# Kernel tuning notes

Measured on AMD Instinct MI355X. Metric: run time of the kernel, lower is better.

The kernel has to match this reference:

```python
import jax, jax.numpy as jnp
import numpy as np

B, N, D, H = 2, 2048, 2048, 16
HD = D // H  # head_dim = 128


def _rope(x, cos, sin):
    # x: [B,H,N,HD]; cos/sin: [N,HD]. use_real=True, use_real_unbind_dim=-1 (interleaved pairs).
    xr = x[..., 0::2]
    xi = x[..., 1::2]
    x_rot = jnp.stack([-xi, xr], axis=-1).reshape(x.shape)
    return x * cos[None, None] + x_rot * sin[None, None]


def setup_inputs() -> dict:
    key = jax.random.key(0)
    ks = jax.random.split(key, 10)
    x = jax.random.normal(ks[0], (B, N, D), dtype=jnp.float32)
    # realistic RoPE tables
    inv_freq = 1.0 / (10000.0 ** (np.arange(0, HD, 2, dtype=np.float32) / HD))
    t = np.arange(N, dtype=np.float32)
    ang = np.einsum('n,f->nf', t, inv_freq)           # [N, HD/2]
    ang = np.repeat(ang, 2, axis=-1)                  # [N, HD] interleaved
    cos = jnp.asarray(np.cos(ang))
    sin = jnp.asarray(np.sin(ang))
    s = 0.02
    Wq = jax.random.normal(ks[1], (D, D), dtype=jnp.float32) * s
    Wk = jax.random.normal(ks[2], (D, D), dtype=jnp.float32) * s
    Wv = jax.random.normal(ks[3], (D, D), dtype=jnp.float32) * s
    Wo = jax.random.normal(ks[4], (D, D), dtype=jnp.float32) * s
    bq = jnp.zeros((D,), jnp.float32)
    bk = jnp.zeros((D,), jnp.float32)
    bv = jnp.zeros((D,), jnp.float32)
    bo = jnp.zeros((D,), jnp.float32)
    return {"x": x, "cos": cos, "sin": sin, "Wq": Wq, "bq": bq, "Wk": Wk,
            "bk": bk, "Wv": Wv, "bv": bv, "Wo": Wo, "bo": bo}


def reference(x, cos, sin, Wq, bq, Wk, bk, Wv, bv, Wo, bo):
    scale = HD ** -0.5
    q = x @ Wq + bq
    k = x @ Wk + bk
    v = x @ Wv + bv
    # b n (h c) -> b h n c
    def split_heads(t):
        return t.reshape(B, N, H, HD).transpose(0, 2, 1, 3)
    q, k, v = split_heads(q), split_heads(k), split_heads(v)
    q = q * scale  # module's dp_scale
    q = _rope(q, cos, sin)
    k = _rope(k, cos, sin)
    # flash_attn_func(softmax_scale=None) applies head_dim^-0.5 AGAIN -> effective HD^-1
    logits = jnp.einsum('bhqc,bhkc->bhqk', q, k) * scale
    attn = jax.nn.softmax(logits, axis=-1)
    o = jnp.einsum('bhqk,bhkc->bhqc', attn, v)
    o = o.transpose(0, 2, 1, 3).reshape(B, N, D)  # b h n c -> b n (h c)
    return o @ Wo + bo
```

## Files before the change

### kernel.cpp

```cpp
#include <hip/hip_runtime.h>

typedef unsigned short u16;
typedef unsigned int u32;
typedef __attribute__((ext_vector_type(8))) short bfx8;
typedef __attribute__((ext_vector_type(4))) float fx4;
typedef __attribute__((ext_vector_type(16))) float fx16;
typedef __attribute__((ext_vector_type(4))) unsigned short u16x4;

#define MFMA_BF16(a,b,c)   __builtin_amdgcn_mfma_f32_16x16x32_bf16((a),(b),(c),0,0,0)
#define MFMA32_BF16(a,b,c) __builtin_amdgcn_mfma_f32_32x32x16_bf16((a),(b),(c),0,0,0)

#define BATCH 2
#define SEQ   2048
#define DM    2048
#define NH    16
#define HD    128
#define MR    4096

__device__ __forceinline__ u16 f2bf(float f){
  union{float f; unsigned u;} v; v.f = f;
  unsigned r = v.u + 0x7FFFu + ((v.u >> 16) & 1u);
  return (u16)(r >> 16);
}
__device__ __forceinline__ unsigned cvtpk(float lo, float hi){
  unsigned r;
  asm("v_cvt_pk_bf16_f32 %0, %1, %2" : "=v"(r) : "v"(lo), "v"(hi));
  return r;
}
__device__ __forceinline__ void gll16(const void* g, void* l){
  __builtin_amdgcn_global_load_lds(
      (const __attribute__((address_space(1))) void*)g,
      (__attribute__((address_space(3))) void*)l, 16, 0, 0);
}

__global__ __launch_bounds__(256) void k_cast(const float* __restrict__ in,
                                              u16* __restrict__ o, int n4){
  int gid = blockIdx.x*256 + threadIdx.x;
  if (gid >= n4) return;
  float4 x = ((const float4*)in)[gid];
  u16x4 v = {f2bf(x.x), f2bf(x.y), f2bf(x.z), f2bf(x.w)};
  ((u16x4*)o)[gid] = v;
}

__global__ __launch_bounds__(256) void k_twcat(const float* __restrict__ Wq,
                                               const float* __restrict__ Wk,
                                               const float* __restrict__ Wv,
                                               u16* __restrict__ Th){
  __shared__ float T[64][65];
  int z = blockIdx.z;
  const float* W = (z==0) ? Wq : (z==1) ? Wk : Wv;
  int n0 = blockIdx.x*64, k0 = blockIdx.y*64;
  int t = threadIdx.x;
  int r = t>>2, c = (t&3)*16;
  const float* src = W + (size_t)(k0+r)*DM + n0 + c;
  #pragma unroll
  for (int j=0;j<4;j++){
    float4 v = *(const float4*)(src + 4*j);
    T[r][c+4*j+0]=v.x; T[r][c+4*j+1]=v.y; T[r][c+4*j+2]=v.z; T[r][c+4*j+3]=v.w;
  }
  __syncthreads();
  int nr = t>>2, kc = (t&3)*16;
  size_t ob = (size_t)(z*DM + n0+nr)*DM + k0 + kc;
  #pragma unroll
  for (int j=0;j<16;j+=4){
    u16x4 vh;
    #pragma unroll
    for (int q=0;q<4;q++) vh[q] = f2bf(T[kc+j+q][nr]);
    *(u16x4*)(Th+ob+j)=vh;
  }
}

__global__ __launch_bounds__(256) void k_tw(const float* __restrict__ W, u16* __restrict__ Th){
  __shared__ float T[64][65];
  int n0 = blockIdx.x*64, k0 = blockIdx.y*64;
  int t = threadIdx.x;
  int r = t>>2, c = (t&3)*16;
  const float* src = W + (size_t)(k0+r)*DM + n0 + c;
  #pragma unroll
  for (int j=0;j<4;j++){
    float4 v = *(const float4*)(src + 4*j);
    T[r][c+4*j+0]=v.x; T[r][c+4*j+1]=v.y; T[r][c+4*j+2]=v.z; T[r][c+4*j+3]=v.w;
  }
  __syncthreads();
  int nr = t>>2, kc = (t&3)*16;
  size_t ob = (size_t)(n0+nr)*DM + k0 + kc;
  #pragma unroll
  for (int j=0;j<16;j+=4){
    u16x4 vh;
    #pragma unroll
    for (int q=0;q<4;q++) vh[q] = f2bf(T[kc+j+q][nr]);
    *(u16x4*)(Th+ob+j)=vh;
  }
}

__global__ __launch_bounds__(256) void k_gemm_qkv(
    const u16* __restrict__ A, const u16* __restrict__ B,
    const float* __restrict__ bqp, const float* __restrict__ bkp, const float* __restrict__ bvp,
    const float* __restrict__ cs, const float* __restrict__ sn,
    u16* __restrict__ qb, u16* __restrict__ kb, u16* __restrict__ vt)
{
  __shared__ u16 sA[128*64], sB[128*64];
  const int K = DM;
  const int tid = threadIdx.x;
  const int lane = tid & 63;
  const int w = tid >> 6;
  const int g = lane >> 4, qi = lane & 15;
  const int wr = w >> 1, wc = w & 1;
  const int bm = blockIdx.y * 128;
  const int bn = blockIdx.x * 128;

  int r_[4], sc_[4];
  #pragma unroll
  for (int i=0;i<4;i++){
    int off = w*4096 + i*1024 + lane*16;
    int r = off>>7, cb = off&127;
    r_[i] = r; sc_[i] = (cb ^ ((r&7)<<4)) >> 1;
  }

  fx4 acc[4][4] = {};

  for (int k0 = 0; k0 < K; k0 += 64){
    __syncthreads();
    #pragma unroll
    for (int i=0;i<4;i++){
      gll16(A + (size_t)(bm + r_[i])*K + k0 + sc_[i], &sA[w*2048 + i*512]);
      gll16(B + (size_t)(bn + r_[i])*K + k0 + sc_[i], &sB[w*2048 + i*512]);
    }
    __syncthreads();

    #pragma unroll
    for (int kk=0;kk<2;kk++){
      const int cb = kk*64 + g*16;
      bfx8 fa[4], fb[4];
      #pragma unroll
      for (int m=0;m<4;m++){
        int row = wr*64 + m*16 + qi;
        fa[m] = *(const bfx8*)((const char*)sA + row*128 + (cb ^ ((row&7)<<4)));
      }
      #pragma unroll
      for (int n=0;n<4;n++){
        int row = wc*64 + n*16 + qi;
        fb[n] = *(const bfx8*)((const char*)sB + row*128 + (cb ^ ((row&7)<<4)));
      }
      #pragma unroll
      for (int m=0;m<4;m++)
        #pragma unroll
        for (int n=0;n<4;n++)
          acc[m][n] = MFMA_BF16(fa[m], fb[n], acc[m][n]);
    }
  }

  const int sec = bn >> 11;
  if (sec < 2){
    u16* dst = sec ? kb : qb;
    const float* bias = sec ? bkp : bqp;
    const float qs = sec ? 1.0f : (1.4426950408889634f/128.0f);
    #pragma unroll
    for (int m=0;m<4;m++){
      #pragma unroll
      for (int n=0;n<4;n++){
        int col = bn + wc*64 + n*16 + qi;
        int cq = col & 2047, hh = cq>>7, d = cq&127;
        float bc = bias[cq];
        float sgn = (d&1) ? 1.0f : -1.0f;
        #pragma unroll
        for (int r=0;r<4;r++){
          int row = bm + wr*64 + m*16 + g*4 + r;
          int bI = row>>11, nr2 = row&2047;
          float v = (acc[m][n][r] + bc)*qs;
          float p = __shfl_xor(v, 1, 64);
          float c = cs[nr2*HD + d], s = sn[nr2*HD + d];
          float y = v*c + sgn*p*s;
          dst[((size_t)(bI*NH+hh)*SEQ + nr2)*HD + d] = f2bf(y);
        }
      }
    }
  } else {
    #pragma unroll
    for (int m=0;m<4;m++){
      #pragma unroll
      for (int n=0;n<4;n++){
        int col = bn + wc*64 + n*16 + qi;
        int cv = col & 2047, hh = cv>>7, d = cv&127;
        float bc = bvp[cv];
        int row0 = bm + wr*64 + m*16 + g*4;
        int bI = row0>>11, n0_ = row0&2047;
        u16x4 pk;
        #pragma unroll
        for (int r=0;r<4;r++) pk[r] = f2bf(acc[m][n][r] + bc);
        *(u16x4*)(vt + ((size_t)(bI*NH+hh)*HD + d)*SEQ + n0_) = pk;
      }
    }
  }
}

__global__ __launch_bounds__(256) void k_gemm(
    const u16* __restrict__ A, const u16* __restrict__ B,
    const float* __restrict__ bias, float* __restrict__ C,
    int M, int N, int K)
{
  __shared__ u16 sA[128*64], sB[128*64];
  const int tid = threadIdx.x;
  const int lane = tid & 63;
  const int w = tid >> 6;
  const int g = lane >> 4, qi = lane & 15;
  const int wr = w >> 1, wc = w & 1;
  const int bm = blockIdx.y * 128;
  const int bn = blockIdx.x * 128;

  int r_[4], sc_[4];
  #pragma unroll
  for (int i=0;i<4;i++){
    int off = w*4096 + i*1024 + lane*16;
    int r = off>>7, cb = off&127;
    r_[i] = r; sc_[i] = (cb ^ ((r&7)<<4)) >> 1;
  }

  fx4 acc[4][4] = {};

  for (int k0 = 0; k0 < K; k0 += 64){
    __syncthreads();
    #pragma unroll
    for (int i=0;i<4;i++){
      gll16(A + (size_t)(bm + r_[i])*K + k0 + sc_[i], &sA[w*2048 + i*512]);
      gll16(B + (size_t)(bn + r_[i])*K + k0 + sc_[i], &sB[w*2048 + i*512]);
    }
    __syncthreads();

    #pragma unroll
    for (int kk=0;kk<2;kk++){
      const int cb = kk*64 + g*16;
      bfx8 fa[4], fb[4];
      #pragma unroll
      for (int m=0;m<4;m++){
        int row = wr*64 + m*16 + qi;
        fa[m] = *(const bfx8*)((const char*)sA + row*128 + (cb ^ ((row&7)<<4)));
      }
      #pragma unroll
      for (int n=0;n<4;n++){
        int row = wc*64 + n*16 + qi;
        fb[n] = *(const bfx8*)((const char*)sB + row*128 + (cb ^ ((row&7)<<4)));
      }
      #pragma unroll
      for (int m=0;m<4;m++)
        #pragma unroll
        for (int n=0;n<4;n++)
          acc[m][n] = MFMA_BF16(fa[m], fb[n], acc[m][n]);
    }
  }

  #pragma unroll
  for (int m=0;m<4;m++){
    #pragma unroll
    for (int n=0;n<4;n++){
      int col = bn + wc*64 + n*16 + qi;
      float bc = bias[col];
      #pragma unroll
      for (int r=0;r<4;r++){
        int row = bm + wr*64 + m*16 + g*4 + r;
        C[(size_t)row*N + col] = acc[m][n][r] + bc;
      }
    }
  }
}

__global__ __launch_bounds__(64) void k_flash(const u16* __restrict__ Q, const u16* __restrict__ Kb,
                                              const u16* __restrict__ Vt, u16* __restrict__ O){
  __shared__ union SM {
    struct { u16 k[64*128]; u16 v[128*64]; } s;
    u16 ob[32*128];
  } sm;
  const int tid = threadIdx.x, lane = tid & 63;
  const int bid0 = blockIdx.x;
  const int bid = ((bid0 & 7) << 8) | (bid0 >> 3);
  const int qt = bid & 63, h = (bid>>6)&15, b = bid>>10;
  const int bh = b*NH + h;
  const int qb0 = qt*32;
  const int hi = lane >> 5, qi = lane & 31;
  const u16* Kb2 = Kb + (size_t)bh*SEQ*HD;
  const u16* Vt2 = Vt + (size_t)bh*SEQ*HD;

  bfx8 qf[8];
  {
    const u16* qp = Q + ((size_t)bh*SEQ + qb0 + qi)*HD + hi*8;
    #pragma unroll
    for (int ks=0; ks<8; ++ks) qf[ks] = *(const bfx8*)(qp + ks*16);
  }

  u32 koff[16], voff[16];
  #pragma unroll
  for (int i=0;i<16;i++){
    int off = i*1024 + lane*16;
    int kr = off>>8, kc = off&255;
    int kcs = kc ^ ((kr&15)<<4);
    koff[i] = kr*HD + (kcs>>1);
    int vr = off>>7, vc = off&127;
    int vcs = vc ^ ((vr&7)<<4);
    voff[i] = vr*SEQ + (vcs>>1);
  }

#define STAGE_K(kv_) do { _Pragma("unroll") \
    for (int i_=0;i_<16;i_++) gll16(Kb2 + koff[i_] + (u32)(kv_)*HD, &sm.s.k[i_*512]); } while(0)
#define STAGE_V(kv_) do { _Pragma("unroll") \
    for (int i_=0;i_<16;i_++) gll16(Vt2 + voff[i_] + (u32)(kv_),    &sm.s.v[i_*512]); } while(0)

  fx16 accO0 = {}, accO1 = {}, accO2 = {}, accO3 = {};
  float mrun = -1e30f, lrun = 0.f;

  STAGE_K(0);
  STAGE_V(0);

  for (int t=0; t<32; ++t){
    asm volatile("s_waitcnt vmcnt(16)" ::: "memory");

    fx16 stA = {}, stB = {};
    #pragma unroll
    for (int ks=0; ks<8; ++ks){
      const int cb = ks*32 + hi*16;
      int rowA = qi;
      int rowB = 32 + qi;
      bfx8 kfa = *(const bfx8*)((const char*)sm.s.k + rowA*256 + (cb ^ ((rowA&15)<<4)));
      bfx8 kfb = *(const bfx8*)((const char*)sm.s.k + rowB*256 + (cb ^ ((rowB&15)<<4)));
      stA = MFMA32_BF16(kfa, qf[ks], stA);
      stB = MFMA32_BF16(kfb, qf[ks], stB);
    }
    asm volatile("s_waitcnt lgkmcnt(0)" ::: "memory");
    if (t < 31) STAGE_K(t*64 + 64);

    float pm = stA[0];
    #pragma unroll
    for (int i=1;i<16;i++) pm = fmaxf(pm, stA[i]);
    #pragma unroll
    for (int i=0;i<16;i++) pm = fmaxf(pm, stB[i]);
    pm = fmaxf(pm, __shfl_xor(pm, 32, 64));
    if (!__all(pm <= mrun + 11.0f)){
      float mn = fmaxf(mrun, pm);
      float al = exp2f(mrun - mn);
      lrun *= al;
      accO0 *= al; accO1 *= al; accO2 *= al; accO3 *= al;
      mrun = mn;
    }
    float ps = 0.f;
    #pragma unroll
    for (int i=0;i<16;i++){
      float p0 = exp2f(stA[i] - mrun); stA[i] = p0; ps += p0;
      float p1 = exp2f(stB[i] - mrun); stB[i] = p1; ps += p1;
    }
    lrun += ps;

    bfx8 pv0, pv1, pv2, pv3;
#define PACK(pvx_, stX_, base_) do { \
      unsigned a0 = cvtpk(stX_[base_+0], stX_[base_+1]); \
      unsigned a1 = cvtpk(stX_[base_+2], stX_[base_+3]); \
      unsigned b0 = cvtpk(stX_[base_+4], stX_[base_+5]); \
      unsigned b1 = cvtpk(stX_[base_+6], stX_[base_+7]); \
      asm volatile("v_permlane32_swap_b32 %0, %1" : "+v"(a0), "+v"(b0)); \
      asm volatile("v_permlane32_swap_b32 %0, %1" : "+v"(a1), "+v"(b1)); \
      union { bfx8 v; unsigned u[4]; } pu_; \
      pu_.u[0] = a0; pu_.u[1] = a1; pu_.u[2] = b0; pu_.u[3] = b1; \
      pvx_ = pu_.v; } while(0)
    PACK(pv0, stA, 0);
    PACK(pv1, stA, 8);
    PACK(pv2, stB, 0);
    PACK(pv3, stB, 8);
#undef PACK

    if (t < 31) asm volatile("s_waitcnt vmcnt(16)" ::: "memory");
    else        asm volatile("s_waitcnt vmcnt(0)"  ::: "memory");

    #pragma unroll
    for (int dblk=0; dblk<4; ++dblk){
      const int row = dblk*32 + qi;
      const int swz = (row&7)<<4;
      const char* vrow = (const char*)sm.s.v + row*128;
      bfx8 vf0 = *(const bfx8*)(vrow + ((0*32 + hi*16) ^ swz));
      bfx8 vf1 = *(const bfx8*)(vrow + ((1*32 + hi*16) ^ swz));
      bfx8 vf2 = *(const bfx8*)(vrow + ((2*32 + hi*16) ^ swz));
      bfx8 vf3 = *(const bfx8*)(vrow + ((3*32 + hi*16) ^ swz));
      fx16 a = (dblk==0)?accO0:(dblk==1)?accO1:(dblk==2)?accO2:accO3;
      a = MFMA32_BF16(vf0, pv0, a);
      a = MFMA32_BF16(vf1, pv1, a);
      a = MFMA32_BF16(vf2, pv2, a);
      a = MFMA32_BF16(vf3, pv3, a);
      if (dblk==0) accO0 = a; else if (dblk==1) accO1 = a; else if (dblk==2) accO2 = a; else accO3 = a;
    }
    asm volatile("s_waitcnt lgkmcnt(0)" ::: "memory");
    if (t < 31) STAGE_V(t*64 + 64);
  }
#undef STAGE_K
#undef STAGE_V

  {
    float l = lrun + __shfl_xor(lrun, 32, 64);
    float inv = 1.0f / l;
    int q = qi;
    char* obr = (char*)sm.ob + q*256;
    const int swz = (q&7)<<4;
#define OWRITE(accX_, dblk_) do { _Pragma("unroll") \
    for (int p=0;p<8;p++){ \
      int d = dblk_*32 + 2*(p&1) + 8*(p>>1) + 4*hi; \
      unsigned wv = cvtpk(accX_[2*p]*inv, accX_[2*p+1]*inv); \
      *(unsigned*)(obr + ((d*2) ^ swz)) = wv; } } while(0)
    OWRITE(accO0, 0); OWRITE(accO1, 1); OWRITE(accO2, 2); OWRITE(accO3, 3);
#undef OWRITE
  }
  __syncthreads();
  {
    int q2 = tid>>1, c0 = (tid&1)*64;
    u16* dst = O + (size_t)(b*SEQ + qb0 + q2)*DM + h*HD + c0;
    #pragma unroll
    for (int jj=0;jj<8;jj++){
      int d0 = c0 + jj*8;
      bfx8 v = *(const bfx8*)((const char*)sm.ob + q2*256 + ((d0*2) ^ ((q2&7)<<4)));
      *(bfx8*)(dst + jj*8) = v;
    }
  }
}

extern "C" void kernel_launch(void* const* d_in, const int* in_sizes, int n_in,
                              void* d_out, int out_size, void* d_ws, size_t ws_size,
                              hipStream_t stream){
  (void)in_sizes; (void)n_in; (void)out_size; (void)ws_size;
  const float* x  = (const float*)d_in[0];
  const float* cs = (const float*)d_in[1];
  const float* sn = (const float*)d_in[2];
  const float* Wq = (const float*)d_in[3];
  const float* bq = (const float*)d_in[4];
  const float* Wk = (const float*)d_in[5];
  const float* bk = (const float*)d_in[6];
  const float* Wv = (const float*)d_in[7];
  const float* bv = (const float*)d_in[8];
  const float* Wo = (const float*)d_in[9];
  const float* bo = (const float*)d_in[10];
  float* out = (float*)d_out;

  char* ws = (char*)d_ws;
  const size_t MB = 1048576;
  u16* xb   = (u16*)(ws);
  u16* wt   = (u16*)(ws + 16*MB);
  u16* qb   = (u16*)(ws + 40*MB);
  u16* kb   = (u16*)(ws + 56*MB);
  u16* vt   = (u16*)(ws + 72*MB);
  u16* ob16 = (u16*)(ws + 88*MB);

  k_cast<<<8192,256,0,stream>>>(x, xb, 2097152);
  k_twcat<<<dim3(32,32,3),256,0,stream>>>(Wq, Wk, Wv, wt);
  k_gemm_qkv<<<dim3(48,32),256,0,stream>>>(xb, wt, bq, bk, bv, cs, sn, qb, kb, vt);

  k_flash<<<2048,64,0,stream>>>(qb, kb, vt, ob16);

  k_tw<<<dim3(32,32),256,0,stream>>>(Wo, wt);
  k_gemm<<<dim3(16,32),256,0,stream>>>(ob16, wt, bo, out, MR, DM, DM);
}
```

Measured before the change: 336.2 us.

## Load K and V fragments directly from global memory in flash kernel

Removes the LDS staging of K and V tiles (async global-to-LDS loads with swizzled offsets and waitcnt pipelining). Each lane now reads its MFMA operand fragments straight from global memory, and the V fragments are prefetched into registers before the softmax step. This frees 32 KB of LDS per block, which may raise occupancy. The cost is that loads no longer overlap across iterations, and it depends on L2 and L1 to serve the reuse.

```diff
diff --git a/kernel.cpp b/kernel.cpp
--- a/kernel.cpp
+++ b/kernel.cpp
@@ -266,10 +266,7 @@
 
 __global__ __launch_bounds__(64) void k_flash(const u16* __restrict__ Q, const u16* __restrict__ Kb,
                                               const u16* __restrict__ Vt, u16* __restrict__ O){
-  __shared__ union SM {
-    struct { u16 k[64*128]; u16 v[128*64]; } s;
-    u16 ob[32*128];
-  } sm;
+  __shared__ u16 ob[32*128];
   const int tid = threadIdx.x, lane = tid & 63;
   const int bid0 = blockIdx.x;
   const int bid = ((bid0 & 7) << 8) | (bid0 >> 3);
@@ -287,45 +284,32 @@
     for (int ks=0; ks<8; ++ks) qf[ks] = *(const bfx8*)(qp + ks*16);
   }
 
-  u32 koff[16], voff[16];
-  #pragma unroll
-  for (int i=0;i<16;i++){
-    int off = i*1024 + lane*16;
-    int kr = off>>8, kc = off&255;
-    int kcs = kc ^ ((kr&15)<<4);
-    koff[i] = kr*HD + (kcs>>1);
-    int vr = off>>7, vc = off&127;
-    int vcs = vc ^ ((vr&7)<<4);
-    voff[i] = vr*SEQ + (vcs>>1);
-  }
-
-#define STAGE_K(kv_) do { _Pragma("unroll") \
-    for (int i_=0;i_<16;i_++) gll16(Kb2 + koff[i_] + (u32)(kv_)*HD, &sm.s.k[i_*512]); } while(0)
-#define STAGE_V(kv_) do { _Pragma("unroll") \
-    for (int i_=0;i_<16;i_++) gll16(Vt2 + voff[i_] + (u32)(kv_),    &sm.s.v[i_*512]); } while(0)
+  const u16* krow = Kb2 + (size_t)qi*HD + hi*8;
+  const u16* vrow = Vt2 + (size_t)qi*SEQ + hi*8;
 
   fx16 accO0 = {}, accO1 = {}, accO2 = {}, accO3 = {};
   float mrun = -1e30f, lrun = 0.f;
 
-  STAGE_K(0);
-  STAGE_V(0);
-
   for (int t=0; t<32; ++t){
-    asm volatile("s_waitcnt vmcnt(16)" ::: "memory");
+    const int kv = t*64;
+    const u16* kp = krow + (size_t)kv*HD;
 
     fx16 stA = {}, stB = {};
     #pragma unroll
     for (int ks=0; ks<8; ++ks){
-      const int cb = ks*32 + hi*16;
-      int rowA = qi;
-      int rowB = 32 + qi;
-      bfx8 kfa = *(const bfx8*)((const char*)sm.s.k + rowA*256 + (cb ^ ((rowA&15)<<4)));
-      bfx8 kfb = *(const bfx8*)((const char*)sm.s.k + rowB*256 + (cb ^ ((rowB&15)<<4)));
+      bfx8 kfa = *(const bfx8*)(kp + ks*16);
+      bfx8 kfb = *(const bfx8*)(kp + 32*HD + ks*16);
       stA = MFMA32_BF16(kfa, qf[ks], stA);
       stB = MFMA32_BF16(kfb, qf[ks], stB);
     }
-    asm volatile("s_waitcnt lgkmcnt(0)" ::: "memory");
-    if (t < 31) STAGE_K(t*64 + 64);
+
+    const u16* vp = vrow + kv;
+    bfx8 vf[4][4];
+    #pragma unroll
+    for (int dblk=0; dblk<4; ++dblk)
+      #pragma unroll
+      for (int ks=0; ks<4; ++ks)
+        vf[dblk][ks] = *(const bfx8*)(vp + (size_t)(dblk*32)*SEQ + ks*16);
 
     float pm = stA[0];
     #pragma unroll
@@ -365,36 +349,29 @@
     PACK(pv3, stB, 8);
 #undef PACK
 
-    if (t < 31) asm volatile("s_waitcnt vmcnt(16)" ::: "memory");
-    else        asm volatile("s_waitcnt vmcnt(0)"  ::: "memory");
-
-    #pragma unroll
-    for (int dblk=0; dblk<4; ++dblk){
-      const int row = dblk*32 + qi;
-      const int swz = (row&7)<<4;
-      const char* vrow = (const char*)sm.s.v + row*128;
-      bfx8 vf0 = *(const bfx8*)(vrow + ((0*32 + hi*16) ^ swz));
-      bfx8 vf1 = *(const bfx8*)(vrow + ((1*32 + hi*16) ^ swz));
-      bfx8 vf2 = *(const bfx8*)(vrow + ((2*32 + hi*16) ^ swz));
-      bfx8 vf3 = *(const bfx8*)(vrow + ((3*32 + hi*16) ^ swz));
-      fx16 a = (dblk==0)?accO0:(dblk==1)?accO1:(dblk==2)?accO2:accO3;
-      a = MFMA32_BF16(vf0, pv0, a);
-      a = MFMA32_BF16(vf1, pv1, a);
-      a = MFMA32_BF16(vf2, pv2, a);
-      a = MFMA32_BF16(vf3, pv3, a);
-      if (dblk==0) accO0 = a; else if (dblk==1) accO1 = a; else if (dblk==2) accO2 = a; else accO3 = a;
-    }
-    asm volatile("s_waitcnt lgkmcnt(0)" ::: "memory");
-    if (t < 31) STAGE_V(t*64 + 64);
-  }
-#undef STAGE_K
-#undef STAGE_V
+    accO0 = MFMA32_BF16(vf[0][0], pv0, accO0);
+    accO0 = MFMA32_BF16(vf[0][1], pv1, accO0);
+    accO0 = MFMA32_BF16(vf[0][2], pv2, accO0);
+    accO0 = MFMA32_BF16(vf[0][3], pv3, accO0);
+    accO1 = MFMA32_BF16(vf[1][0], pv0, accO1);
+    accO1 = MFMA32_BF16(vf[1][1], pv1, accO1);
+    accO1 = MFMA32_BF16(vf[1][2], pv2, accO1);
+    accO1 = MFMA32_BF16(vf[1][3], pv3, accO1);
+    accO2 = MFMA32_BF16(vf[2][0], pv0, accO2);
+    accO2 = MFMA32_BF16(vf[2][1], pv1, accO2);
+    accO2 = MFMA32_BF16(vf[2][2], pv2, accO2);
+    accO2 = MFMA32_BF16(vf[2][3], pv3, accO2);
+    accO3 = MFMA32_BF16(vf[3][0], pv0, accO3);
+    accO3 = MFMA32_BF16(vf[3][1], pv1, accO3);
+    accO3 = MFMA32_BF16(vf[3][2], pv2, accO3);
+    accO3 = MFMA32_BF16(vf[3][3], pv3, accO3);
+  }
 
   {
     float l = lrun + __shfl_xor(lrun, 32, 64);
     float inv = 1.0f / l;
     int q = qi;
-    char* obr = (char*)sm.ob + q*256;
+    char* obr = (char*)ob + q*256;
     const int swz = (q&7)<<4;
 #define OWRITE(accX_, dblk_) do { _Pragma("unroll") \
     for (int p=0;p<8;p++){ \
@@ -411,7 +388,7 @@
     #pragma unroll
     for (int jj=0;jj<8;jj++){
       int d0 = c0 + jj*8;
-      bfx8 v = *(const bfx8*)((const char*)sm.ob + q2*256 + ((d0*2) ^ ((q2&7)<<4)));
+      bfx8 v = *(const bfx8*)((const char*)ob + q2*256 + ((d0*2) ^ ((q2&7)<<4)));
       *(bfx8*)(dst + jj*8) = v;
     }
   }
```

After: 427.0 us. 1.27x slower.
